# Optimization experiments

Hardware: AMD Instinct MI355X
Metric: run time of the kernel (lower is better)

Reference implementation:

```python
import jax, jax.numpy as jnp
import numpy as np

H = 64        # num_attention_heads
HK = 8        # num_key_value_heads
HD = 64       # head_dim
DM = 1024     # hidden_size
WINDOW = 128  # sliding_window


def setup_inputs() -> dict:
    key = jax.random.key(0)
    ks = jax.random.split(key, 9)
    B, S = 2, 1024
    s = 0.02
    return {
        "x": jax.random.normal(ks[0], (B, S, DM), jnp.float32),
        "Wq": jax.random.normal(ks[1], (H * HD, DM), jnp.float32) * s,
        "bq": jax.random.normal(ks[2], (H * HD,), jnp.float32) * s,
        "Wk": jax.random.normal(ks[3], (HK * HD, DM), jnp.float32) * s,
        "bk": jax.random.normal(ks[4], (HK * HD,), jnp.float32) * s,
        "Wv": jax.random.normal(ks[5], (HK * HD, DM), jnp.float32) * s,
        "bv": jax.random.normal(ks[6], (HK * HD,), jnp.float32) * s,
        "Wo": jax.random.normal(ks[7], (DM, H * HD), jnp.float32) * s,
        "bo": jax.random.normal(ks[8], (DM,), jnp.float32) * s,
        "sinks": jnp.ones((H,), jnp.float32),
    }


def reference(x, Wq, bq, Wk, bk, Wv, bv, Wo, bo, sinks):
    B, S, _ = x.shape
    G = H // HK  # GQA group size

    q = (x @ Wq.T + bq).reshape(B, S, H, HD).transpose(0, 2, 1, 3)    # [B,H,S,hd]
    k = (x @ Wk.T + bk).reshape(B, S, HK, HD).transpose(0, 2, 1, 3)   # [B,Hk,S,hd]
    v = (x @ Wv.T + bv).reshape(B, S, HK, HD).transpose(0, 2, 1, 3)
    k = jnp.repeat(k, G, axis=1)  # [B,H,S,hd]
    v = jnp.repeat(v, G, axis=1)

    scale = 1.0 / np.sqrt(HD).astype(np.float32)
    scores = jnp.einsum("bhqd,bhkd->bhqk", q, k) * scale  # [B,H,S,S]

    # causal + sliding-window mask: attend iff 0 <= q_pos - k_pos < WINDOW
    qi = jnp.arange(S)[:, None]
    kj = jnp.arange(S)[None, :]
    allowed = (qi >= kj) & (qi - kj < WINDOW)             # [S,S]
    neg = jnp.asarray(-1e30, scores.dtype)
    scores = jnp.where(allowed[None, None], scores, neg)

    # per-head learned sink logit appended as an extra softmax column
    sink = jnp.broadcast_to(sinks[None, :, None, None], (B, H, S, 1))
    logits = jnp.concatenate([scores, sink], axis=-1)      # [B,H,S,S+1]
    probs = jax.nn.softmax(logits, axis=-1)[..., :-1]      # drop sink column

    o = jnp.einsum("bhqk,bhkd->bhqd", probs, v)            # [B,H,S,hd]
    o = o.transpose(0, 2, 1, 3).reshape(B, S, H * HD)
    return o @ Wo.T + bo                                   # [B,S,DM]
```

## Files before the change

kernel.cpp:

```cpp
#include <hip/hip_runtime.h>
#include <math.h>

#define H 64
#define HK 8
#define HD 64
#define DM 1024
#define WINDOW 128
#define GQA (H / HK)
#define Bv 2
#define Sv 1024

typedef _Float16 f16;
typedef __attribute__((ext_vector_type(8))) _Float16 f16x8;
typedef __attribute__((ext_vector_type(4))) _Float16 f16x4;
typedef __attribute__((ext_vector_type(4))) float f32x4;

__device__ __forceinline__ void gload_lds16(const void* g, void* l) {
    __builtin_amdgcn_global_load_lds((const __attribute__((address_space(1))) void*)g,
                                     (__attribute__((address_space(3))) void*)l, 16, 0, 0);
}

__global__ __launch_bounds__(256, 2) void qkv_gemm(const f16* __restrict__ xh,
                                                   const f16* __restrict__ wqkv,
                                                   const float* __restrict__ bqkv,
                                                   f16* __restrict__ qh,
                                                   f16* __restrict__ khb,
                                                   f16* __restrict__ vtb) {
    __shared__ __align__(16) f16 As[128 * 64];
    __shared__ __align__(16) f16 Bs[160 * 64];

    const int t    = threadIdx.x;
    const int lane = t & 63;
    const int w    = t >> 6;
    const int lr   = lane & 15;
    const int quad = lane >> 4;
    const int srow = lane >> 3;
    const int gsw  = lane & 7;
    const int bx   = blockIdx.x & 31;
    const int by   = blockIdx.x >> 5;
    const int m0   = by * 128;
    const int n0   = bx * 160;
    const int wm   = w >> 1;
    const int wn   = w & 1;

    f32x4 acc[4][5] = {};

    for (int k0 = 0; k0 < DM; k0 += 64) {
#pragma unroll
        for (int i = 0; i < 4; ++i) {
            const int row = (w * 4 + i) * 8 + srow;
            const int g   = gsw ^ (row & 7);
            gload_lds16(xh + (size_t)(m0 + row) * DM + k0 + g * 8, As + (w * 4 + i) * 512);
        }
#pragma unroll
        for (int i = 0; i < 5; ++i) {
            const int row = (w * 5 + i) * 8 + srow;
            const int g   = gsw ^ (row & 7);
            gload_lds16(wqkv + (size_t)(n0 + row) * DM + k0 + g * 8, Bs + (w * 5 + i) * 512);
        }
        __syncthreads();
#pragma unroll
        for (int ks = 0; ks < 2; ++ks) {
            f16x8 af[4], bf[5];
#pragma unroll
            for (int tt = 0; tt < 4; ++tt) {
                const int m  = wm * 64 + tt * 16 + lr;
                const int ca = (ks * 4 + quad) ^ (m & 7);
                af[tt] = *(const f16x8*)(As + m * 64 + ca * 8);
            }
#pragma unroll
            for (int tt = 0; tt < 5; ++tt) {
                const int n  = wn * 80 + tt * 16 + lr;
                const int cb = (ks * 4 + quad) ^ (n & 7);
                bf[tt] = *(const f16x8*)(Bs + n * 64 + cb * 8);
            }
#pragma unroll
            for (int i = 0; i < 4; ++i)
#pragma unroll
                for (int j = 0; j < 5; ++j)
                    acc[i][j] = __builtin_amdgcn_mfma_f32_16x16x32_f16(af[i], bf[j], acc[i][j], 0, 0, 0);
        }
        __syncthreads();
    }

#pragma unroll
    for (int i = 0; i < 4; ++i) {
        const int grow = m0 + wm * 64 + i * 16 + quad * 4;
#pragma unroll
        for (int j = 0; j < 5; ++j) {
            const int gcb  = n0 + wn * 80 + j * 16;
            const int gcol = gcb + lr;
            const float bz = bqkv[gcol];
            if (gcb < 4096) {
#pragma unroll
                for (int r = 0; r < 4; ++r)
                    qh[(size_t)(grow + r) * 4096 + gcol] = (f16)((acc[i][j][r] + bz) * 0.125f);
            } else if (gcb < 4608) {
                const int lc = gcol - 4096;
                const size_t base = (size_t)(grow >> 10) * 524288 + (size_t)(lc >> 6) * 65536
                                  + (size_t)(grow & 1023) * 64 + (lc & 63);
#pragma unroll
                for (int r = 0; r < 4; ++r)
                    khb[base + (size_t)r * 64] = (f16)(acc[i][j][r] + bz);
            } else {
                const int lc = gcol - 4608;
                const size_t base = ((size_t)(grow >> 10) * 512 + lc) * 1024 + (grow & 1023);
                f16x4 o;
#pragma unroll
                for (int r = 0; r < 4; ++r) o[r] = (f16)(acc[i][j][r] + bz);
                *(f16x4*)(vtb + base) = o;
            }
        }
    }
}

__global__ __launch_bounds__(256, 2) void o_gemm_split(const f16* __restrict__ oh,
                                                       const f16* __restrict__ woh,
                                                       float* __restrict__ partials) {
    __shared__ __align__(16) f16 As[128 * 64];
    __shared__ __align__(16) f16 Bs[128 * 64];

    const int t    = threadIdx.x;
    const int lane = t & 63;
    const int w    = t >> 6;
    const int lr   = lane & 15;
    const int quad = lane >> 4;
    const int srow = lane >> 3;
    const int gsw  = lane & 7;
    const int kz   = blockIdx.z;
    const int m0   = blockIdx.y * 128;
    const int n0   = blockIdx.x * 128;
    const int wm   = w >> 1;
    const int wn   = w & 1;

    const f16* A = oh  + (size_t)kz * 1024;
    const f16* W = woh + (size_t)kz * 1024;
    float* P = partials + (size_t)kz * 2097152;

    f32x4 acc[4][4] = {};

    for (int k0 = 0; k0 < 1024; k0 += 64) {
#pragma unroll
        for (int i = 0; i < 4; ++i) {
            const int row = (w * 4 + i) * 8 + srow;
            const int g   = gsw ^ (row & 7);
            gload_lds16(A + (size_t)(m0 + row) * 4096 + k0 + g * 8, As + (w * 4 + i) * 512);
            gload_lds16(W + (size_t)(n0 + row) * 4096 + k0 + g * 8, Bs + (w * 4 + i) * 512);
        }
        __syncthreads();
#pragma unroll
        for (int ks = 0; ks < 2; ++ks) {
            f16x8 af[4], bf[4];
#pragma unroll
            for (int tt = 0; tt < 4; ++tt) {
                const int m  = wm * 64 + tt * 16 + lr;
                const int ca = (ks * 4 + quad) ^ (m & 7);
                af[tt] = *(const f16x8*)(As + m * 64 + ca * 8);
                const int n  = wn * 64 + tt * 16 + lr;
                const int cb = (ks * 4 + quad) ^ (n & 7);
                bf[tt] = *(const f16x8*)(Bs + n * 64 + cb * 8);
            }
#pragma unroll
            for (int i = 0; i < 4; ++i)
#pragma unroll
                for (int j = 0; j < 4; ++j)
                    acc[i][j] = __builtin_amdgcn_mfma_f32_16x16x32_f16(af[i], bf[j], acc[i][j], 0, 0, 0);
        }
        __syncthreads();
    }

#pragma unroll
    for (int i = 0; i < 4; ++i) {
        const int grow = m0 + wm * 64 + i * 16 + quad * 4;
#pragma unroll
        for (int j = 0; j < 4; ++j) {
            const int gcol = n0 + wn * 64 + j * 16 + lr;
#pragma unroll
            for (int r = 0; r < 4; ++r)
                P[(size_t)(grow + r) * 1024 + gcol] = acc[i][j][r];
        }
    }
}

__global__ __launch_bounds__(256) void reduce4(const float* __restrict__ partials,
                                               const float* __restrict__ bo,
                                               float* __restrict__ out) {
    const int i = blockIdx.x * 256 + threadIdx.x;
    const float4* p = (const float4*)partials;
    float4 a  = p[i];
    float4 b1 = p[i + 524288], b2 = p[i + 1048576], b3 = p[i + 1572864];
    float4 bz = ((const float4*)bo)[i & 255];
    float4 o;
    o.x = a.x + b1.x + b2.x + b3.x + bz.x;
    o.y = a.y + b1.y + b2.y + b3.y + bz.y;
    o.z = a.z + b1.z + b2.z + b3.z + bz.z;
    o.w = a.w + b1.w + b2.w + b3.w + bz.w;
    ((float4*)out)[i] = o;
}

#define C_X  524288
#define C_WQ 1572864
#define C_WK 1703936
#define C_WV 1835008
#define C_WO 2883584

__global__ __launch_bounds__(256) void convert_all(const float* __restrict__ x,
                                                   const float* __restrict__ Wq,
                                                   const float* __restrict__ Wk,
                                                   const float* __restrict__ Wv,
                                                   const float* __restrict__ Wo,
                                                   const float* __restrict__ bq,
                                                   const float* __restrict__ bk,
                                                   const float* __restrict__ bv,
                                                   f16* __restrict__ xh,
                                                   f16* __restrict__ wqkv,
                                                   f16* __restrict__ woh,
                                                   float* __restrict__ bqkv) {
    const int i = blockIdx.x * 256 + threadIdx.x;
    if (i < 5120) {
        float v;
        if (i < 4096)      v = bq[i];
        else if (i < 4608) v = bk[i - 4096];
        else               v = bv[i - 4608];
        bqkv[i] = v;
    }
    const float* src;
    f16* dst;
    int off;
    if (i < C_X)       { src = x;  dst = xh;              off = i; }
    else if (i < C_WQ) { src = Wq; dst = wqkv;            off = i - C_X; }
    else if (i < C_WK) { src = Wk; dst = wqkv + 4194304;  off = i - C_WQ; }
    else if (i < C_WV) { src = Wv; dst = wqkv + 4718592;  off = i - C_WK; }
    else               { src = Wo; dst = woh;             off = i - C_WV; }
    const float4 v = ((const float4*)src)[off];
    f16x4 o;
    o[0] = (f16)v.x; o[1] = (f16)v.y; o[2] = (f16)v.z; o[3] = (f16)v.w;
    *(f16x4*)(dst + (size_t)off * 4) = o;
}

#define KT 192
#define KLS 72
#define VTS 200
#define PLS 200

__global__ __launch_bounds__(256) void attn_mfma(const f16* __restrict__ qh,
                                                 const f16* __restrict__ khb,
                                                 const f16* __restrict__ vtb,
                                                 const float* __restrict__ sinks,
                                                 f16* __restrict__ oh) {
    __shared__ __align__(16) f16 Kl[KT * KLS];
    __shared__ __align__(16) f16 Vt[HD * VTS];
    __shared__ __align__(16) f16 Pl[4 * 16 * PLS];

    const int t  = threadIdx.x;
    const int q0 = blockIdx.x * 64;
    const int hk = blockIdx.y >> 1;
    const int hh = blockIdx.y & 1;
    const int b  = blockIdx.z;
    const int c0 = q0 - WINDOW;

    const f16* kg = khb + (size_t)(b * HK + hk) * Sv * HD;
    const f16* vg = vtb + (size_t)(b * HK + hk) * HD * Sv;

#pragma unroll
    for (int ii = 0; ii < 6; ++ii) {
        const int i = ii * 256 + t;
        const int slot = i >> 3, c = i & 7;
        const int j = c0 + slot;
        f16x8 val = {};
        if (j >= 0) val = *(const f16x8*)(kg + (size_t)j * HD + c * 8);
        *(f16x8*)(&Kl[slot * KLS + c * 8]) = val;
    }
#pragma unroll
    for (int ii = 0; ii < 6; ++ii) {
        const int i = ii * 256 + t;
        const int d = i / 24, c = i % 24;
        const int j0 = c0 + c * 8;
        f16x8 val = {};
        if (j0 >= 0) val = *(const f16x8*)(vg + (size_t)d * Sv + j0);
        *(f16x8*)(&Vt[d * VTS + c * 8]) = val;
    }
    __syncthreads();

    const int lane = t & 63;
    const int w    = t >> 6;
    const int h    = hk * GQA + hh * 4 + w;
    const int lr   = lane & 15;
    const int quad = lane >> 4;
    f16* Pw = Pl + w * 16 * PLS;

    f16x8 qf[4][2];
#pragma unroll
    for (int mt = 0; mt < 4; ++mt) {
        const int q = q0 + mt * 16 + lr;
        const f16* qrow = qh + (size_t)(b * Sv + q) * (H * HD) + h * HD;
#pragma unroll
        for (int ks = 0; ks < 2; ++ks)
            qf[mt][ks] = *(const f16x8*)(qrow + ks * 32 + quad * 8);
    }
    const float sk   = sinks[h];
    const int   smin = (c0 < 0) ? -c0 : 0;

#pragma unroll
    for (int mt = 0; mt < 4; ++mt) {
        f32x4 S[12];
#pragma unroll
        for (int nt = 0; nt < 12; ++nt) {
            f32x4 a = {};
#pragma unroll
            for (int ks = 0; ks < 2; ++ks) {
                f16x8 bfr = *(const f16x8*)(&Kl[(nt * 16 + lr) * KLS + ks * 32 + quad * 8]);
                a = __builtin_amdgcn_mfma_f32_16x16x32_f16(qf[mt][ks], bfr, a, 0, 0, 0);
            }
            S[nt] = a;
        }
        float rmax[4] = {-1e30f, -1e30f, -1e30f, -1e30f};
#pragma unroll
        for (int nt = 0; nt < 12; ++nt) {
            const int sl = nt * 16 + lr;
#pragma unroll
            for (int r = 0; r < 4; ++r) {
                const int mq = mt * 16 + quad * 4 + r;
                const bool ok = (sl > mq) && (sl <= mq + WINDOW) && (sl >= smin);
                const float v = ok ? S[nt][r] : -INFINITY;
                S[nt][r] = v;
                rmax[r] = fmaxf(rmax[r], v);
            }
        }
#pragma unroll
        for (int off = 1; off < 16; off <<= 1)
#pragma unroll
            for (int r = 0; r < 4; ++r)
                rmax[r] = fmaxf(rmax[r], __shfl_xor(rmax[r], off, 64));
        float mrow[4], lsum[4];
#pragma unroll
        for (int r = 0; r < 4; ++r) { mrow[r] = fmaxf(rmax[r], sk); lsum[r] = 0.f; }
#pragma unroll
        for (int nt = 0; nt < 12; ++nt) {
#pragma unroll
            for (int r = 0; r < 4; ++r) {
                const float p = __expf(S[nt][r] - mrow[r]);
                lsum[r] += p;
                Pw[(quad * 4 + r) * PLS + nt * 16 + lr] = (f16)p;
            }
        }
#pragma unroll
        for (int off = 1; off < 16; off <<= 1)
#pragma unroll
            for (int r = 0; r < 4; ++r)
                lsum[r] += __shfl_xor(lsum[r], off, 64);
        float inv[4];
#pragma unroll
        for (int r = 0; r < 4; ++r)
            inv[r] = 1.f / (lsum[r] + __expf(sk - mrow[r]));
        f32x4 O[4] = {};
#pragma unroll
        for (int kc = 0; kc < 6; ++kc) {
            const f16x8 pa = *(const f16x8*)(&Pw[lr * PLS + kc * 32 + quad * 8]);
#pragma unroll
            for (int dt = 0; dt < 4; ++dt) {
                const f16x8 vf = *(const f16x8*)(&Vt[(dt * 16 + lr) * VTS + kc * 32 + quad * 8]);
                O[dt] = __builtin_amdgcn_mfma_f32_16x16x32_f16(pa, vf, O[dt], 0, 0, 0);
            }
        }
#pragma unroll
        for (int dt = 0; dt < 4; ++dt) {
#pragma unroll
            for (int r = 0; r < 4; ++r) {
                const int q = q0 + mt * 16 + quad * 4 + r;
                oh[(size_t)(b * Sv + q) * (H * HD) + h * HD + dt * 16 + lr] =
                    (f16)(O[dt][r] * inv[r]);
            }
        }
    }
}

extern "C" void kernel_launch(void* const* d_in, const int* in_sizes, int n_in,
                              void* d_out, int out_size, void* d_ws, size_t ws_size,
                              hipStream_t stream) {
    const float* x     = (const float*)d_in[0];
    const float* Wq    = (const float*)d_in[1];
    const float* bq    = (const float*)d_in[2];
    const float* Wk    = (const float*)d_in[3];
    const float* bk    = (const float*)d_in[4];
    const float* Wv    = (const float*)d_in[5];
    const float* bv    = (const float*)d_in[6];
    const float* Wo    = (const float*)d_in[7];
    const float* bo    = (const float*)d_in[8];
    const float* sinks = (const float*)d_in[9];
    float* out = (float*)d_out;

    f16* xh   = (f16*)d_ws;
    f16* wqkv = xh + 2097152;
    f16* qh   = wqkv + 5242880;
    f16* khb  = qh + 8388608;
    f16* vtb  = khb + 1048576;
    f16* woh  = vtb + 1048576;
    f16* oh   = woh + 4194304;
    float* bqkv = (float*)(oh + 8388608);
    float* partials = (float*)d_ws;

    convert_all<<<dim3(C_WO / 256), dim3(256), 0, stream>>>(
        x, Wq, Wk, Wv, Wo, bq, bk, bv, xh, wqkv, woh, bqkv);

    qkv_gemm<<<dim3(512), dim3(256), 0, stream>>>(xh, wqkv, bqkv, qh, khb, vtb);

    attn_mfma<<<dim3(Sv / 64, HK * 2, Bv), dim3(256), 0, stream>>>(qh, khb, vtb, sinks, oh);

    o_gemm_split<<<dim3(8, 16, 4), dim3(256), 0, stream>>>(oh, woh, partials);
    reduce4<<<dim3(2048), dim3(256), 0, stream>>>(partials, bo, out);
}
```

Baseline: 182.6 us.

## Fuse softmax into PV MFMA via transposed scores, skip masked tiles

Computes scores as K·Q^T so probabilities stay in registers in the operand layout for a 16x16x16 MFMA with V^T. This removes the LDS staging of P and the row-max reduction. Fully masked 16x16 tiles are skipped, K is loaded directly to LDS with an XOR swizzle, and output stores are vectorised. Omitting max subtraction risks exp overflow for large logits, and occupancy is raised via launch bounds.

```diff
diff --git a/kernel.cpp b/kernel.cpp
--- a/kernel.cpp
+++ b/kernel.cpp
@@ -238,19 +238,15 @@
     *(f16x4*)(dst + (size_t)off * 4) = o;
 }
 
-#define KT 192
-#define KLS 72
 #define VTS 200
-#define PLS 200
-
-__global__ __launch_bounds__(256) void attn_mfma(const f16* __restrict__ qh,
-                                                 const f16* __restrict__ khb,
-                                                 const f16* __restrict__ vtb,
-                                                 const float* __restrict__ sinks,
-                                                 f16* __restrict__ oh) {
-    __shared__ __align__(16) f16 Kl[KT * KLS];
-    __shared__ __align__(16) f16 Vt[HD * VTS];
-    __shared__ __align__(16) f16 Pl[4 * 16 * PLS];
+
+__global__ __launch_bounds__(256, 3) void attn_mfma(const f16* __restrict__ qh,
+                                                    const f16* __restrict__ khb,
+                                                    const f16* __restrict__ vtb,
+                                                    const float* __restrict__ sinks,
+                                                    f16* __restrict__ oh) {
+    __shared__ __align__(16) f16 Kl[192 * 64];
+    __shared__ __align__(16) f16 Vt[64 * VTS];
 
     const int t  = threadIdx.x;
     const int q0 = blockIdx.x * 64;
@@ -259,41 +255,41 @@
     const int b  = blockIdx.z;
     const int c0 = q0 - WINDOW;
 
+    const int lane = t & 63;
+    const int w    = t >> 6;
+    const int lr   = lane & 15;
+    const int quad = lane >> 4;
+    const int srow = lane >> 3;
+    const int gsw  = lane & 7;
+
     const f16* kg = khb + (size_t)(b * HK + hk) * Sv * HD;
     const f16* vg = vtb + (size_t)(b * HK + hk) * HD * Sv;
 
 #pragma unroll
-    for (int ii = 0; ii < 6; ++ii) {
-        const int i = ii * 256 + t;
-        const int slot = i >> 3, c = i & 7;
-        const int j = c0 + slot;
-        f16x8 val = {};
-        if (j >= 0) val = *(const f16x8*)(kg + (size_t)j * HD + c * 8);
-        *(f16x8*)(&Kl[slot * KLS + c * 8]) = val;
-    }
-#pragma unroll
-    for (int ii = 0; ii < 6; ++ii) {
-        const int i = ii * 256 + t;
+    for (int it = 0; it < 6; ++it) {
+        const int row = (w * 6 + it) * 8 + srow;
+        const int g   = gsw ^ (row & 7);
+        int j = c0 + row;
+        if (j < 0) j = 0;
+        gload_lds16(kg + (size_t)j * HD + g * 8, Kl + (w * 6 + it) * 512);
+    }
+#pragma unroll
+    for (int it = 0; it < 6; ++it) {
+        const int i = it * 256 + t;
         const int d = i / 24, c = i % 24;
-        const int j0 = c0 + c * 8;
-        f16x8 val = {};
-        if (j0 >= 0) val = *(const f16x8*)(vg + (size_t)d * Sv + j0);
+        int j0 = c0 + c * 8;
+        if (j0 < 0) j0 = 0;
+        const f16x8 val = *(const f16x8*)(vg + (size_t)d * Sv + j0);
         *(f16x8*)(&Vt[d * VTS + c * 8]) = val;
     }
     __syncthreads();
 
-    const int lane = t & 63;
-    const int w    = t >> 6;
-    const int h    = hk * GQA + hh * 4 + w;
-    const int lr   = lane & 15;
-    const int quad = lane >> 4;
-    f16* Pw = Pl + w * 16 * PLS;
+    const int h = hk * GQA + hh * 4 + w;
 
     f16x8 qf[4][2];
 #pragma unroll
     for (int mt = 0; mt < 4; ++mt) {
-        const int q = q0 + mt * 16 + lr;
-        const f16* qrow = qh + (size_t)(b * Sv + q) * (H * HD) + h * HD;
+        const f16* qrow = qh + (size_t)(b * Sv + q0 + mt * 16 + lr) * 4096 + h * 64;
 #pragma unroll
         for (int ks = 0; ks < 2; ++ks)
             qf[mt][ks] = *(const f16x8*)(qrow + ks * 32 + quad * 8);
@@ -301,76 +297,62 @@
     const float sk   = sinks[h];
     const int   smin = (c0 < 0) ? -c0 : 0;
 
+    f32x4 O[4][4] = {};
+    float lsum[4] = {0.f, 0.f, 0.f, 0.f};
+
+#pragma unroll
+    for (int nt = 0; nt < 12; ++nt) {
+        f16x8 kf[2];
+#pragma unroll
+        for (int ks = 0; ks < 2; ++ks)
+            kf[ks] = *(const f16x8*)(&Kl[(nt * 16 + lr) * 64 + (((ks * 4 + quad) ^ (lr & 7)) * 8)]);
+        f16x4 vf[4];
+#pragma unroll
+        for (int dt = 0; dt < 4; ++dt)
+            vf[dt] = *(const f16x4*)(&Vt[(dt * 16 + lr) * VTS + nt * 16 + quad * 4]);
+
+#pragma unroll
+        for (int mt = 0; mt < 4; ++mt) {
+            if (nt < mt || nt > mt + 8) continue;
+            f32x4 S = {};
+#pragma unroll
+            for (int ks = 0; ks < 2; ++ks)
+                S = __builtin_amdgcn_mfma_f32_16x16x32_f16(kf[ks], qf[mt][ks], S, 0, 0, 0);
+            f16x4 pf;
+#pragma unroll
+            for (int r = 0; r < 4; ++r) {
+                const int sl = nt * 16 + quad * 4 + r;
+                const int mq = mt * 16 + lr;
+                const bool ok = (sl > mq) && (sl <= mq + WINDOW) && (sl >= smin);
+                const float p = ok ? __expf(S[r]) : 0.f;
+                lsum[mt] += p;
+                pf[r] = (f16)p;
+            }
+#pragma unroll
+            for (int dt = 0; dt < 4; ++dt)
+                O[mt][dt] = __builtin_amdgcn_mfma_f32_16x16x16f16(vf[dt], pf, O[mt][dt], 0, 0, 0);
+        }
+    }
+
+    const float esk = __expf(sk);
 #pragma unroll
     for (int mt = 0; mt < 4; ++mt) {
-        f32x4 S[12];
-#pragma unroll
-        for (int nt = 0; nt < 12; ++nt) {
-            f32x4 a = {};
-#pragma unroll
-            for (int ks = 0; ks < 2; ++ks) {
-                f16x8 bfr = *(const f16x8*)(&Kl[(nt * 16 + lr) * KLS + ks * 32 + quad * 8]);
-                a = __builtin_amdgcn_mfma_f32_16x16x32_f16(qf[mt][ks], bfr, a, 0, 0, 0);
-            }
-            S[nt] = a;
-        }
-        float rmax[4] = {-1e30f, -1e30f, -1e30f, -1e30f};
-#pragma unroll
-        for (int nt = 0; nt < 12; ++nt) {
-            const int sl = nt * 16 + lr;
-#pragma unroll
-            for (int r = 0; r < 4; ++r) {
-                const int mq = mt * 16 + quad * 4 + r;
-                const bool ok = (sl > mq) && (sl <= mq + WINDOW) && (sl >= smin);
-                const float v = ok ? S[nt][r] : -INFINITY;
-                S[nt][r] = v;
-                rmax[r] = fmaxf(rmax[r], v);
-            }
-        }
-#pragma unroll
-        for (int off = 1; off < 16; off <<= 1)
-#pragma unroll
-            for (int r = 0; r < 4; ++r)
-                rmax[r] = fmaxf(rmax[r], __shfl_xor(rmax[r], off, 64));
-        float mrow[4], lsum[4];
-#pragma unroll
-        for (int r = 0; r < 4; ++r) { mrow[r] = fmaxf(rmax[r], sk); lsum[r] = 0.f; }
-#pragma unroll
-        for (int nt = 0; nt < 12; ++nt) {
-#pragma unroll
-            for (int r = 0; r < 4; ++r) {
-                const float p = __expf(S[nt][r] - mrow[r]);
-                lsum[r] += p;
-                Pw[(quad * 4 + r) * PLS + nt * 16 + lr] = (f16)p;
-            }
-        }
-#pragma unroll
-        for (int off = 1; off < 16; off <<= 1)
-#pragma unroll
-            for (int r = 0; r < 4; ++r)
-                lsum[r] += __shfl_xor(lsum[r], off, 64);
-        float inv[4];
-#pragma unroll
-        for (int r = 0; r < 4; ++r)
-            inv[r] = 1.f / (lsum[r] + __expf(sk - mrow[r]));
-        f32x4 O[4] = {};
-#pragma unroll
-        for (int kc = 0; kc < 6; ++kc) {
-            const f16x8 pa = *(const f16x8*)(&Pw[lr * PLS + kc * 32 + quad * 8]);
-#pragma unroll
-            for (int dt = 0; dt < 4; ++dt) {
-                const f16x8 vf = *(const f16x8*)(&Vt[(dt * 16 + lr) * VTS + kc * 32 + quad * 8]);
-                O[dt] = __builtin_amdgcn_mfma_f32_16x16x32_f16(pa, vf, O[dt], 0, 0, 0);
-            }
-        }
+        float l = lsum[mt];
+        l += __shfl_xor(l, 16, 64);
+        l += __shfl_xor(l, 32, 64);
+        lsum[mt] = 1.f / (l + esk);
+    }
+
+#pragma unroll
+    for (int mt = 0; mt < 4; ++mt) {
+        const float inv = lsum[mt];
+        f16* orow = oh + (size_t)(b * Sv + q0 + mt * 16 + lr) * 4096 + h * 64;
 #pragma unroll
         for (int dt = 0; dt < 4; ++dt) {
-#pragma unroll
-            for (int r = 0; r < 4; ++r) {
-                const int q = q0 + mt * 16 + quad * 4 + r;
-                oh[(size_t)(b * Sv + q) * (H * HD) + h * HD + dt * 16 + lr] =
-                    (f16)(O[dt][r] * inv[r]);
-            }
+            f16x4 ov;
+#pragma unroll
+            for (int r = 0; r < 4; ++r) ov[r] = (f16)(O[mt][dt][r] * inv);
+            *(f16x4*)(orow + dt * 16 + quad * 4) = ov;
         }
     }
 }
```

Result: slower. 201.6 us (+10.4%).
